# Optimization experiments

Hardware: AMD Instinct MI355X
Metric: run time of the kernel (lower is better)

## Reference

```python
import jax, jax.numpy as jnp
import numpy as np

D_MODEL = 1024
D_STATE = 16
EXPAND = 2
D_INNER = D_MODEL * EXPAND
DT_RANK = D_MODEL // 16


def setup_inputs() -> dict:
    key = jax.random.key(0)
    ks = jax.random.split(key, 12)
    B, T = 2, 2048
    s_in = 1.0 / np.sqrt(D_MODEL)
    s_x = 1.0 / np.sqrt(D_INNER)
    s_dt = 1.0 / np.sqrt(DT_RANK)
    inp = {
        'u': jax.random.normal(ks[0], (B, T, D_MODEL), jnp.float32),
        'W_in': jax.random.uniform(ks[1], (2 * D_INNER, D_MODEL), jnp.float32, -s_in, s_in),
        'b_in': jax.random.uniform(ks[2], (2 * D_INNER,), jnp.float32, -s_in, s_in),
        'W_x': jax.random.uniform(ks[3], (DT_RANK + 2 * D_STATE, D_INNER), jnp.float32, -s_x, s_x),
        'b_x': jax.random.uniform(ks[4], (DT_RANK + 2 * D_STATE,), jnp.float32, -s_x, s_x),
        'W_dt': jax.random.uniform(ks[5], (D_INNER, DT_RANK), jnp.float32, -s_dt, s_dt),
        'b_dt': jax.random.uniform(ks[6], (D_INNER,), jnp.float32, -s_dt, s_dt),
        'A_log': jnp.log(jnp.abs(jax.random.normal(ks[7], (D_INNER, D_STATE), jnp.float32)) + 1e-6),
        'D': jnp.ones((D_INNER,), jnp.float32),
        'W_out': jax.random.uniform(ks[8], (D_MODEL, D_INNER), jnp.float32, -s_x, s_x),
        'b_out': jax.random.uniform(ks[9], (D_MODEL,), jnp.float32, -s_x, s_x),
    }
    return inp


def _ssm_forward(u, W_in, b_in, W_x, b_x, W_dt, b_dt, A_log, D, W_out, b_out):
    B, T, _ = u.shape
    u_inner = u @ W_in.T + b_in                       # [B,T,2*d_inner]
    x, z = jnp.split(u_inner, 2, axis=-1)             # each [B,T,d_inner]
    dbc = x @ W_x.T + b_x                             # [B,T,dt_rank+2N]
    delta_raw = dbc[..., :DT_RANK]
    B_ssm = dbc[..., DT_RANK:DT_RANK + D_STATE]       # [B,T,N]
    C_ssm = dbc[..., DT_RANK + D_STATE:]              # [B,T,N]
    delta = jax.nn.softplus(delta_raw @ W_dt.T + b_dt)  # [B,T,d_inner]
    A = -jnp.exp(A_log)                               # [d_inner,N]

    def step(h, xs):
        dt_t, x_t, Bt, Ct = xs                        # [B,d], [B,d], [B,N], [B,N]
        dA = jnp.exp(dt_t[..., None] * A)             # [B,d,N]
        dB = dt_t[..., None] * Bt[:, None, :]         # [B,d,N]
        h = h * dA + x_t[..., None] * dB
        y_t = jnp.einsum('bdn,bn->bd', h, Ct)
        return h, y_t

    h0 = jnp.zeros((B, D_INNER, D_STATE), u.dtype)
    xs = (jnp.swapaxes(delta, 0, 1), jnp.swapaxes(x, 0, 1),
          jnp.swapaxes(B_ssm, 0, 1), jnp.swapaxes(C_ssm, 0, 1))
    _, y = jax.lax.scan(step, h0, xs)                 # y: [T,B,d_inner]
    y = jnp.swapaxes(y, 0, 1)                         # [B,T,d_inner]
    y = y + x * D
    y = y * (z * jax.nn.sigmoid(z))                   # SiLU gate
    return y @ W_out.T + b_out                        # [B,T,d_model]


def reference(u, W_in, b_in, W_x, b_x, W_dt, b_dt, A_log, D, W_out, b_out):
    return _ssm_forward(u, W_in, b_in, W_x, b_x, W_dt, b_dt, A_log, D, W_out, b_out)
```

## Files before the change

### kernel.cpp

```cpp
#include <hip/hip_runtime.h>
#include <math.h>

#define BATCH 2
#define SEQ   2048
#define DM    1024
#define DI    2048
#define NST   16
#define MT    (BATCH*SEQ)
#define CHK   64
#define LCH   (SEQ/CHK)

typedef __attribute__((ext_vector_type(8))) short  bf16x8;
typedef __attribute__((ext_vector_type(4))) float  f32x4;

static __device__ __forceinline__ unsigned short f2bf(float f) {
  unsigned u = __float_as_uint(f);
  u += 0x7fff + ((u >> 16) & 1);
  return (unsigned short)(u >> 16);
}
static __device__ __forceinline__ float bf2f(unsigned short h) {
  return __uint_as_float(((unsigned)h) << 16);
}
static __device__ __forceinline__ float fexp2(float x) {
  float r;
  asm("v_exp_f32 %0, %1" : "=v"(r) : "v"(x));
  return r;
}
static __device__ __forceinline__ float flog2(float x) {
  float r;
  asm("v_log_f32 %0, %1" : "=v"(r) : "v"(x));
  return r;
}

__global__ __launch_bounds__(256) void conv_bf16_kernel(
    const float* __restrict__ src, unsigned short* __restrict__ dst, int n4)
{
  int i = blockIdx.x * 256 + threadIdx.x;
  if (i < n4) {
    float4 v = ((const float4*)src)[i];
    ushort4 o;
    o.x = f2bf(v.x); o.y = f2bf(v.y); o.z = f2bf(v.z); o.w = f2bf(v.w);
    ((ushort4*)dst)[i] = o;
  }
}

__global__ __launch_bounds__(256) void a2tab_kernel(
    const float* __restrict__ A_log, float* __restrict__ A2tab)
{
  int i = blockIdx.x * 256 + threadIdx.x;
  float4 v = ((const float4*)A_log)[i];
  float4 o;
  o.x = -1.44269504f * __expf(v.x);
  o.y = -1.44269504f * __expf(v.y);
  o.z = -1.44269504f * __expf(v.z);
  o.w = -1.44269504f * __expf(v.w);
  ((float4*)A2tab)[i] = o;
}

template<int BN, bool OUT_BF16, int LDC, int ACT>
__global__ __launch_bounds__(256, 2) void gemm2_kernel(
    const unsigned short* __restrict__ A,
    const unsigned short* __restrict__ B,
    const float* __restrict__ bias,
    void* __restrict__ Cout, int K, int nbx)
{
  constexpr int NJ = BN / 32;
  __shared__ unsigned short Abuf[2][2][128*32];
  __shared__ unsigned short Bbuf[2][2][BN*32];

  const int nwg = gridDim.x;
  const int cpx = nwg >> 3;
  const int bid = blockIdx.x;
  const int swz = (bid & 7) * cpx + (bid >> 3);
  const int bx = swz % nbx;
  const int by = swz / nbx;

  const int tid  = threadIdx.x;
  const int lane = tid & 63;
  const int wid  = tid >> 6;
  const int wr   = wid >> 1;
  const int wc   = wid & 1;
  const int lr    = lane >> 2;
  const int lslot = lane & 3;

  f32x4 zero = {0.f, 0.f, 0.f, 0.f};
  f32x4 acc[4][NJ];
#pragma unroll
  for (int i = 0; i < 4; ++i)
#pragma unroll
    for (int j = 0; j < NJ; ++j) acc[i][j] = zero;

  const size_t arow0 = (size_t)by * 128;
  const size_t brow0 = (size_t)bx * BN;
  const int NT = K >> 6;

  auto STAGE = [&](int buf, int k0) {
#pragma unroll
    for (int half = 0; half < 2; ++half) {
#pragma unroll
      for (int i = 0; i < 2; ++i) {
        const int Rb = (wid + i*4) * 16;
        const int r  = Rb + lr;
        const int c8 = lslot ^ ((r >> 1) & 3);
        const unsigned short* ga = A + (arow0 + r)*(size_t)K + k0 + half*32 + c8*8;
        __builtin_amdgcn_global_load_lds(
            (const __attribute__((address_space(1))) void*)ga,
            (__attribute__((address_space(3))) void*)(&Abuf[buf][half][Rb*32]),
            16, 0, 0);
      }
#pragma unroll
      for (int i = 0; i < BN/64; ++i) {
        const int Rb = (wid + i*4) * 16;
        const int r  = Rb + lr;
        const int c8 = lslot ^ ((r >> 1) & 3);
        const unsigned short* gb = B + (brow0 + r)*(size_t)K + k0 + half*32 + c8*8;
        __builtin_amdgcn_global_load_lds(
            (const __attribute__((address_space(1))) void*)gb,
            (__attribute__((address_space(3))) void*)(&Bbuf[buf][half][Rb*32]),
            16, 0, 0);
      }
    }
  };

  STAGE(0, 0);
  __syncthreads();

  const int lrow = lane & 15, k8 = lane >> 4;
  int cur = 0;
  for (int kt = 0; kt < NT; ++kt) {
    if (kt + 1 < NT) STAGE(cur ^ 1, (kt + 1) * 64);

#pragma unroll
    for (int half = 0; half < 2; ++half) {
      bf16x8 af[4], bfr[NJ];
#pragma unroll
      for (int mi = 0; mi < 4; ++mi) {
        const int r = wr*64 + mi*16 + lrow;
        af[mi] = *(const bf16x8*)&Abuf[cur][half][r*32 + (k8 ^ ((r >> 1) & 3))*8];
      }
#pragma unroll
      for (int nj = 0; nj < NJ; ++nj) {
        const int r = wc*(BN/2) + nj*16 + lrow;
        bfr[nj] = *(const bf16x8*)&Bbuf[cur][half][r*32 + (k8 ^ ((r >> 1) & 3))*8];
      }
      __builtin_amdgcn_s_setprio(1);
#pragma unroll
      for (int mi = 0; mi < 4; ++mi)
#pragma unroll
        for (int nj = 0; nj < NJ; ++nj)
          acc[mi][nj] = __builtin_amdgcn_mfma_f32_16x16x32_bf16(
                            af[mi], bfr[nj], acc[mi][nj], 0, 0, 0);
      __builtin_amdgcn_s_setprio(0);
    }
    __syncthreads();
    cur ^= 1;
  }

  const int lcol = lane & 15, lrq = lane >> 4;
#pragma unroll
  for (int nj = 0; nj < NJ; ++nj) {
    const int colg = bx*BN + wc*(BN/2) + nj*16 + lcol;
    const float bv = bias[colg];
#pragma unroll
    for (int mi = 0; mi < 4; ++mi) {
      const int rowg = by*128 + wr*64 + mi*16 + lrq*4;
#pragma unroll
      for (int q = 0; q < 4; ++q) {
        float v = acc[mi][nj][q] + bv;
        if constexpr (ACT == 1) {
          float e = fexp2(-1.44269504f * fabsf(v));
          v = fmaxf(v, 0.f) + 0.69314718f * flog2(1.f + e);
        }
        if constexpr (OUT_BF16)
          ((unsigned short*)Cout)[(size_t)(rowg + q)*LDC + colg] = f2bf(v);
        else
          ((float*)Cout)[(size_t)(rowg + q)*LDC + colg] = v;
      }
    }
  }
}

__global__ __launch_bounds__(256) void dbc_mfma_kernel(
    const unsigned short* __restrict__ A,
    const unsigned short* __restrict__ Bw,
    const float* __restrict__ bx,
    float* __restrict__ dbc,
    unsigned short* __restrict__ draw_bf)
{
  __shared__ unsigned short Abuf[64*32];
  __shared__ unsigned short Bbuf[96*32];

  const int tid  = threadIdx.x;
  const int lane = tid & 63;
  const int wid  = tid >> 6;
  const int lr    = lane >> 2;
  const int lslot = lane & 3;
  const size_t arow0 = (size_t)blockIdx.x * 64;

  f32x4 zero = {0.f, 0.f, 0.f, 0.f};
  f32x4 acc[6];
#pragma unroll
  for (int j = 0; j < 6; ++j) acc[j] = zero;

  for (int k0 = 0; k0 < DI; k0 += 32) {
    {
      const int Rb = wid*16;
      const int r  = Rb + lr;
      const int c8 = lslot ^ ((r >> 1) & 3);
      const unsigned short* ga = A + (arow0 + r)*4096 + k0 + c8*8;
      __builtin_amdgcn_global_load_lds(
          (const __attribute__((address_space(1))) void*)ga,
          (__attribute__((address_space(3))) void*)(Abuf + Rb*32), 16, 0, 0);
    }
    if (wid < 3) {
#pragma unroll
      for (int i = 0; i < 2; ++i) {
        const int Rb = wid*32 + i*16;
        const int r  = Rb + lr;
        const int c8 = lslot ^ ((r >> 1) & 3);
        const unsigned short* gb = Bw + (size_t)r*DI + k0 + c8*8;
        __builtin_amdgcn_global_load_lds(
            (const __attribute__((address_space(1))) void*)gb,
            (__attribute__((address_space(3))) void*)(Bbuf + Rb*32), 16, 0, 0);
      }
    }
    __syncthreads();

    const int lrow = lane & 15, k8 = lane >> 4;
    const int ra = wid*16 + lrow;
    bf16x8 af = *(const bf16x8*)&Abuf[ra*32 + (k8 ^ ((ra >> 1) & 3))*8];
#pragma unroll
    for (int nj = 0; nj < 6; ++nj) {
      const int rb = nj*16 + lrow;
      bf16x8 bf_ = *(const bf16x8*)&Bbuf[rb*32 + (k8 ^ ((rb >> 1) & 3))*8];
      acc[nj] = __builtin_amdgcn_mfma_f32_16x16x32_bf16(af, bf_, acc[nj], 0, 0, 0);
    }
    __syncthreads();
  }

  const int lcol = lane & 15, lrq = lane >> 4;
  const int rowg = (int)arow0 + wid*16 + lrq*4;
#pragma unroll
  for (int nj = 0; nj < 6; ++nj) {
    const int colg = nj*16 + lcol;
    const float bv = bx[colg];
#pragma unroll
    for (int q = 0; q < 4; ++q) {
      float v = acc[nj][q] + bv;
      if (nj < 4)
        draw_bf[(size_t)(rowg + q)*64 + colg] = f2bf(v);
      else
        dbc[(size_t)(rowg + q)*96 + colg] = v;
    }
  }
}

__global__ __launch_bounds__(256) void scanA_kernel(
    const unsigned short* __restrict__ uib,
    const float* __restrict__ dbc,
    const unsigned short* __restrict__ delta_bf,
    const float* __restrict__ A2tab,
    float* __restrict__ P,
    float* __restrict__ S)
{
  const int bid = blockIdx.x;
  const int d   = (bid & 7)*256 + threadIdx.x;
  const int c   = (bid >> 3) & (CHK-1);
  const int b   = bid >> 9;

  float A2[NST];
  {
    const float4* ap = (const float4*)(A2tab + (size_t)d*NST);
#pragma unroll
    for (int q = 0; q < 4; ++q) {
      float4 v = ap[q];
      A2[q*4+0] = v.x; A2[q*4+1] = v.y; A2[q*4+2] = v.z; A2[q*4+3] = v.w;
    }
  }

  float h[NST];
#pragma unroll
  for (int nn = 0; nn < NST; ++nn) h[nn] = 0.f;
  float sdt = 0.f;

  const int t0 = c * LCH;
  const unsigned short* dptr = delta_bf + ((size_t)b*SEQ + t0)*DI + d;
  const unsigned short* xptr = uib      + ((size_t)b*SEQ + t0)*4096 + d;
  const float* bptr          = dbc      + ((size_t)b*SEQ + t0)*96 + 64;

  float dt = bf2f(dptr[0]);
  float xv = bf2f(xptr[0]);
  float4 Bv0 = *(const float4*)(bptr + 0);
  float4 Bv1 = *(const float4*)(bptr + 4);
  float4 Bv2 = *(const float4*)(bptr + 8);
  float4 Bv3 = *(const float4*)(bptr + 12);

  for (int t = 0; t < LCH; ++t) {
    const float dtc = dt, xvc = xv;
    float Bc[NST] = {Bv0.x,Bv0.y,Bv0.z,Bv0.w, Bv1.x,Bv1.y,Bv1.z,Bv1.w,
                     Bv2.x,Bv2.y,Bv2.z,Bv2.w, Bv3.x,Bv3.y,Bv3.z,Bv3.w};
    if (t + 1 < LCH) {
      const size_t tn = (size_t)(t+1);
      dt = bf2f(dptr[tn*DI]);
      xv = bf2f(xptr[tn*4096]);
      const float* bp = bptr + tn*96;
      Bv0 = *(const float4*)(bp + 0);
      Bv1 = *(const float4*)(bp + 4);
      Bv2 = *(const float4*)(bp + 8);
      Bv3 = *(const float4*)(bp + 12);
    }
    sdt += dtc;
    const float xdt = xvc * dtc;
#pragma unroll
    for (int nn = 0; nn < NST; ++nn) {
      float dA = fexp2(dtc * A2[nn]);
      h[nn] = h[nn]*dA + xdt*Bc[nn];
    }
  }

  float* Pp = P + (((size_t)b*CHK + c)*DI + d)*NST;
  float* Sp = S + (((size_t)b*CHK + c)*DI + d)*NST;
#pragma unroll
  for (int q = 0; q < 4; ++q) {
    float4 pv = { fexp2(A2[q*4+0]*sdt), fexp2(A2[q*4+1]*sdt),
                  fexp2(A2[q*4+2]*sdt), fexp2(A2[q*4+3]*sdt) };
    float4 sv = { h[q*4+0], h[q*4+1], h[q*4+2], h[q*4+3] };
    *(float4*)(Pp + q*4) = pv;
    *(float4*)(Sp + q*4) = sv;
  }
}

__global__ __launch_bounds__(256) void scanB_kernel(
    const float* __restrict__ P, float* __restrict__ S)
{
  const int gid = blockIdx.x*256 + threadIdx.x;
  const int n4 = gid & 3;
  const int d  = (gid >> 2) & (DI-1);
  const int b  = gid >> 13;

  float4 h = {0.f, 0.f, 0.f, 0.f};
  for (int c = 0; c < CHK; ++c) {
    const size_t idx = (((size_t)b*CHK + c)*DI + d)*NST + n4*4;
    float4 p = *(const float4*)(P + idx);
    float4 s = *(const float4*)(S + idx);
    *(float4*)(S + idx) = h;
    h.x = h.x*p.x + s.x;
    h.y = h.y*p.y + s.y;
    h.z = h.z*p.z + s.z;
    h.w = h.w*p.w + s.w;
  }
}

__global__ __launch_bounds__(256) void scanC_kernel(
    const unsigned short* __restrict__ uib,
    const float* __restrict__ dbc,
    const unsigned short* __restrict__ delta_bf,
    const float* __restrict__ A2tab,
    const float* __restrict__ Dp,
    const float* __restrict__ S,
    unsigned short* __restrict__ y_bf)
{
  const int bid = blockIdx.x;
  const int d   = (bid & 7)*256 + threadIdx.x;
  const int c   = (bid >> 3) & (CHK-1);
  const int b   = bid >> 9;

  float A2[NST];
  {
    const float4* ap = (const float4*)(A2tab + (size_t)d*NST);
#pragma unroll
    for (int q = 0; q < 4; ++q) {
      float4 v = ap[q];
      A2[q*4+0] = v.x; A2[q*4+1] = v.y; A2[q*4+2] = v.z; A2[q*4+3] = v.w;
    }
  }
  const float Dv = Dp[d];

  float h[NST];
  {
    const float* Sp = S + (((size_t)b*CHK + c)*DI + d)*NST;
#pragma unroll
    for (int q = 0; q < 4; ++q) {
      float4 sv = *(const float4*)(Sp + q*4);
      h[q*4+0] = sv.x; h[q*4+1] = sv.y; h[q*4+2] = sv.z; h[q*4+3] = sv.w;
    }
  }

  const int t0 = c * LCH;
  const unsigned short* dptr = delta_bf + ((size_t)b*SEQ + t0)*DI + d;
  const unsigned short* xptr = uib      + ((size_t)b*SEQ + t0)*4096 + d;
  const float* cptr          = dbc      + ((size_t)b*SEQ + t0)*96;
  unsigned short* yp         = y_bf     + ((size_t)b*SEQ + t0)*DI + d;

  float dt = bf2f(dptr[0]);
  float xv = bf2f(xptr[0]);
  float zv = bf2f(xptr[2048]);
  float4 Bv0 = *(const float4*)(cptr + 64);
  float4 Bv1 = *(const float4*)(cptr + 68);
  float4 Bv2 = *(const float4*)(cptr + 72);
  float4 Bv3 = *(const float4*)(cptr + 76);
  float4 Cv0 = *(const float4*)(cptr + 80);
  float4 Cv1 = *(const float4*)(cptr + 84);
  float4 Cv2 = *(const float4*)(cptr + 88);
  float4 Cv3 = *(const float4*)(cptr + 92);

  for (int t = 0; t < LCH; ++t) {
    const float dtc = dt, xvc = xv, zvc = zv;
    float Bc[NST] = {Bv0.x,Bv0.y,Bv0.z,Bv0.w, Bv1.x,Bv1.y,Bv1.z,Bv1.w,
                     Bv2.x,Bv2.y,Bv2.z,Bv2.w, Bv3.x,Bv3.y,Bv3.z,Bv3.w};
    float Cc[NST] = {Cv0.x,Cv0.y,Cv0.z,Cv0.w, Cv1.x,Cv1.y,Cv1.z,Cv1.w,
                     Cv2.x,Cv2.y,Cv2.z,Cv2.w, Cv3.x,Cv3.y,Cv3.z,Cv3.w};
    if (t + 1 < LCH) {
      const size_t tn = (size_t)(t+1);
      dt = bf2f(dptr[tn*DI]);
      xv = bf2f(xptr[tn*4096]);
      zv = bf2f(xptr[tn*4096 + 2048]);
      const float* cp = cptr + tn*96;
      Bv0 = *(const float4*)(cp + 64);
      Bv1 = *(const float4*)(cp + 68);
      Bv2 = *(const float4*)(cp + 72);
      Bv3 = *(const float4*)(cp + 76);
      Cv0 = *(const float4*)(cp + 80);
      Cv1 = *(const float4*)(cp + 84);
      Cv2 = *(const float4*)(cp + 88);
      Cv3 = *(const float4*)(cp + 92);
    }
    const float xdt = xvc * dtc;
    float y = 0.f;
#pragma unroll
    for (int nn = 0; nn < NST; ++nn) {
      float dA = fexp2(dtc * A2[nn]);
      h[nn] = h[nn]*dA + xdt*Bc[nn];
      y += h[nn]*Cc[nn];
    }
    y += xvc * Dv;
    y *= zvc / (1.f + fexp2(-1.44269504f * zvc));
    yp[(size_t)t*DI] = f2bf(y);
  }
}

extern "C" void kernel_launch(void* const* d_in, const int* in_sizes, int n_in,
                              void* d_out, int out_size, void* d_ws, size_t ws_size,
                              hipStream_t stream)
{
  const float* u     = (const float*)d_in[0];
  const float* W_in  = (const float*)d_in[1];
  const float* b_in  = (const float*)d_in[2];
  const float* W_x   = (const float*)d_in[3];
  const float* b_x   = (const float*)d_in[4];
  const float* W_dt  = (const float*)d_in[5];
  const float* b_dt  = (const float*)d_in[6];
  const float* A_log = (const float*)d_in[7];
  const float* Dp    = (const float*)d_in[8];
  const float* W_out = (const float*)d_in[9];
  const float* b_out = (const float*)d_in[10];
  float* out = (float*)d_out;

  unsigned short* ui_bf    = (unsigned short*)d_ws;
  float*          dbc      = (float*)(ui_bf + (size_t)MT*4096);
  unsigned short* delta_bf = (unsigned short*)(dbc + (size_t)MT*96);
  unsigned short* y_bf     = delta_bf + (size_t)MT*DI;
  unsigned short* wout_bf  = y_bf + (size_t)MT*DI;
  unsigned short* wx_bf    = wout_bf + (size_t)DM*DI;
  unsigned short* wdt_bf   = wx_bf + (size_t)96*DI;
  unsigned short* draw_bf  = wdt_bf + (size_t)DI*64;
  float*          S        = (float*)(draw_bf + (size_t)MT*64);
  float*          A2tab    = S + (size_t)BATCH*CHK*DI*NST;

  unsigned short* u_bf   = (unsigned short*)d_out;
  unsigned short* win_bf = u_bf + (size_t)MT*DM;
  float* P = (float*)d_out;

  conv_bf16_kernel<<<4096, 256, 0, stream>>>(u,     u_bf,    MT*DM/4);
  conv_bf16_kernel<<<4096, 256, 0, stream>>>(W_in,  win_bf,  2*DI*DM/4);
  conv_bf16_kernel<<<2048, 256, 0, stream>>>(W_out, wout_bf, DM*DI/4);
  conv_bf16_kernel<<<192,  256, 0, stream>>>(W_x,   wx_bf,   96*DI/4);
  conv_bf16_kernel<<<128,  256, 0, stream>>>(W_dt,  wdt_bf,  DI*64/4);
  a2tab_kernel<<<DI*NST/1024, 256, 0, stream>>>(A_log, A2tab);

  gemm2_kernel<128, true, 4096, 0><<<32*32, 256, 0, stream>>>(
      u_bf, win_bf, b_in, ui_bf, DM, 32);

  dbc_mfma_kernel<<<MT/64, 256, 0, stream>>>(ui_bf, wx_bf, b_x, dbc, draw_bf);

  gemm2_kernel<128, true, 2048, 1><<<16*32, 256, 0, stream>>>(
      draw_bf, wdt_bf, b_dt, delta_bf, 64, 16);

  scanA_kernel<<<BATCH*CHK*DI/256, 256, 0, stream>>>(ui_bf, dbc, delta_bf, A2tab, P, S);
  scanB_kernel<<<BATCH*DI*4/256, 256, 0, stream>>>(P, S);
  scanC_kernel<<<BATCH*CHK*DI/256, 256, 0, stream>>>(ui_bf, dbc, delta_bf, A2tab, Dp, S, y_bf);

  gemm2_kernel<64, false, 1024, 0><<<16*32, 256, 0, stream>>>(
      y_bf, wout_bf, b_out, out, DI, 16);
}
```

Baseline: 215.4 us.

## Fuse conversion kernels, split-K the dbc GEMM, and tune GEMM K-tile and occupancy

The five bf16 conversion launches and the A2 table launch are merged into one kernel that branches on a global index range. The dbc projection GEMM is split four ways along K into a partial buffer, followed by a reduce kernel that adds the bias and writes the outputs, so more workgroups run. The generic GEMM gains a BK template parameter: the in-projection and delta GEMMs use BK=32 to shrink shared memory, and launch bounds rise to 4 waves per SIMD. This trades an extra launch and a partial-sum round trip for more parallelism, and risks register spills from the tighter occupancy bound.

```diff
diff --git a/kernel.cpp b/kernel.cpp
--- a/kernel.cpp
+++ b/kernel.cpp
@@ -32,41 +32,62 @@
   return r;
 }
 
-__global__ __launch_bounds__(256) void conv_bf16_kernel(
-    const float* __restrict__ src, unsigned short* __restrict__ dst, int n4)
-{
-  int i = blockIdx.x * 256 + threadIdx.x;
-  if (i < n4) {
-    float4 v = ((const float4*)src)[i];
-    ushort4 o;
-    o.x = f2bf(v.x); o.y = f2bf(v.y); o.z = f2bf(v.z); o.w = f2bf(v.w);
-    ((ushort4*)dst)[i] = o;
-  }
-}
-
-__global__ __launch_bounds__(256) void a2tab_kernel(
-    const float* __restrict__ A_log, float* __restrict__ A2tab)
-{
-  int i = blockIdx.x * 256 + threadIdx.x;
-  float4 v = ((const float4*)A_log)[i];
-  float4 o;
-  o.x = -1.44269504f * __expf(v.x);
-  o.y = -1.44269504f * __expf(v.y);
-  o.z = -1.44269504f * __expf(v.z);
-  o.w = -1.44269504f * __expf(v.w);
-  ((float4*)A2tab)[i] = o;
-}
-
-template<int BN, bool OUT_BF16, int LDC, int ACT>
-__global__ __launch_bounds__(256, 2) void gemm2_kernel(
+#define SEG_U    (MT*DM/4)
+#define SEG_WIN  (2*DI*DM/4)
+#define SEG_WOUT (DM*DI/4)
+#define SEG_WX   (96*DI/4)
+#define SEG_WDT  (DI*64/4)
+#define SEG_A    (DI*NST/4)
+#define CUM0 SEG_U
+#define CUM1 (CUM0+SEG_WIN)
+#define CUM2 (CUM1+SEG_WOUT)
+#define CUM3 (CUM2+SEG_WX)
+#define CUM4 (CUM3+SEG_WDT)
+#define CUM5 (CUM4+SEG_A)
+
+__global__ __launch_bounds__(256) void convall_kernel(
+    const float* __restrict__ u, const float* __restrict__ W_in,
+    const float* __restrict__ W_out, const float* __restrict__ W_x,
+    const float* __restrict__ W_dt, const float* __restrict__ A_log,
+    unsigned short* __restrict__ u_bf, unsigned short* __restrict__ win_bf,
+    unsigned short* __restrict__ wout_bf, unsigned short* __restrict__ wx_bf,
+    unsigned short* __restrict__ wdt_bf, float* __restrict__ A2tab)
+{
+  const int gid = blockIdx.x*256 + threadIdx.x;
+  const float4* src; ushort4* dst; int idx;
+  if (gid < CUM0)      { idx = gid;        src = (const float4*)u;     dst = (ushort4*)u_bf; }
+  else if (gid < CUM1) { idx = gid - CUM0; src = (const float4*)W_in;  dst = (ushort4*)win_bf; }
+  else if (gid < CUM2) { idx = gid - CUM1; src = (const float4*)W_out; dst = (ushort4*)wout_bf; }
+  else if (gid < CUM3) { idx = gid - CUM2; src = (const float4*)W_x;   dst = (ushort4*)wx_bf; }
+  else if (gid < CUM4) { idx = gid - CUM3; src = (const float4*)W_dt;  dst = (ushort4*)wdt_bf; }
+  else if (gid < CUM5) {
+    int i = gid - CUM4;
+    float4 v = ((const float4*)A_log)[i];
+    float4 o;
+    o.x = -1.44269504f * __expf(v.x);
+    o.y = -1.44269504f * __expf(v.y);
+    o.z = -1.44269504f * __expf(v.z);
+    o.w = -1.44269504f * __expf(v.w);
+    ((float4*)A2tab)[i] = o;
+    return;
+  } else return;
+  float4 v = src[idx];
+  ushort4 o;
+  o.x = f2bf(v.x); o.y = f2bf(v.y); o.z = f2bf(v.z); o.w = f2bf(v.w);
+  dst[idx] = o;
+}
+
+template<int BN, int BK, bool OUT_BF16, int LDC, int ACT>
+__global__ __launch_bounds__(256, 4) void gemm2_kernel(
     const unsigned short* __restrict__ A,
     const unsigned short* __restrict__ B,
     const float* __restrict__ bias,
     void* __restrict__ Cout, int K, int nbx)
 {
+  constexpr int NH = BK / 32;
   constexpr int NJ = BN / 32;
-  __shared__ unsigned short Abuf[2][2][128*32];
-  __shared__ unsigned short Bbuf[2][2][BN*32];
+  __shared__ unsigned short Abuf[2][NH][128*32];
+  __shared__ unsigned short Bbuf[2][NH][BN*32];
 
   const int nwg = gridDim.x;
   const int cpx = nwg >> 3;
@@ -92,11 +113,11 @@
 
   const size_t arow0 = (size_t)by * 128;
   const size_t brow0 = (size_t)bx * BN;
-  const int NT = K >> 6;
+  const int NT = K / BK;
 
   auto STAGE = [&](int buf, int k0) {
 #pragma unroll
-    for (int half = 0; half < 2; ++half) {
+    for (int half = 0; half < NH; ++half) {
 #pragma unroll
       for (int i = 0; i < 2; ++i) {
         const int Rb = (wid + i*4) * 16;
@@ -128,10 +149,10 @@
   const int lrow = lane & 15, k8 = lane >> 4;
   int cur = 0;
   for (int kt = 0; kt < NT; ++kt) {
-    if (kt + 1 < NT) STAGE(cur ^ 1, (kt + 1) * 64);
-
-#pragma unroll
-    for (int half = 0; half < 2; ++half) {
+    if (kt + 1 < NT) STAGE(cur ^ 1, (kt + 1) * BK);
+
+#pragma unroll
+    for (int half = 0; half < NH; ++half) {
       bf16x8 af[4], bfr[NJ];
 #pragma unroll
       for (int mi = 0; mi < 4; ++mi) {
@@ -183,9 +204,7 @@
 __global__ __launch_bounds__(256) void dbc_mfma_kernel(
     const unsigned short* __restrict__ A,
     const unsigned short* __restrict__ Bw,
-    const float* __restrict__ bx,
-    float* __restrict__ dbc,
-    unsigned short* __restrict__ draw_bf)
+    float* __restrict__ partial)
 {
   __shared__ unsigned short Abuf[64*32];
   __shared__ unsigned short Bbuf[96*32];
@@ -196,13 +215,15 @@
   const int lr    = lane >> 2;
   const int lslot = lane & 3;
   const size_t arow0 = (size_t)blockIdx.x * 64;
+  const int ks   = blockIdx.y;
+  const int k0b  = ks * (DI/4);
 
   f32x4 zero = {0.f, 0.f, 0.f, 0.f};
   f32x4 acc[6];
 #pragma unroll
   for (int j = 0; j < 6; ++j) acc[j] = zero;
 
-  for (int k0 = 0; k0 < DI; k0 += 32) {
+  for (int k0 = k0b; k0 < k0b + DI/4; k0 += 32) {
     {
       const int Rb = wid*16;
       const int r  = Rb + lr;
@@ -243,16 +264,24 @@
 #pragma unroll
   for (int nj = 0; nj < 6; ++nj) {
     const int colg = nj*16 + lcol;
-    const float bv = bx[colg];
-#pragma unroll
-    for (int q = 0; q < 4; ++q) {
-      float v = acc[nj][q] + bv;
-      if (nj < 4)
-        draw_bf[(size_t)(rowg + q)*64 + colg] = f2bf(v);
-      else
-        dbc[(size_t)(rowg + q)*96 + colg] = v;
-    }
-  }
+#pragma unroll
+    for (int q = 0; q < 4; ++q)
+      partial[((size_t)ks*MT + rowg + q)*96 + colg] = acc[nj][q];
+  }
+}
+
+__global__ __launch_bounds__(256) void dbc_reduce_kernel(
+    const float* __restrict__ partial, const float* __restrict__ bx,
+    float* __restrict__ dbc, unsigned short* __restrict__ draw_bf)
+{
+  const int gid = blockIdx.x*256 + threadIdx.x;
+  const int m = gid / 96;
+  const int c = gid - m*96;
+  const size_t stride = (size_t)MT*96;
+  float s = partial[gid] + partial[gid + stride]
+          + partial[gid + 2*stride] + partial[gid + 3*stride] + bx[c];
+  if (c < 64) draw_bf[(size_t)m*64 + c] = f2bf(s);
+  else        dbc[(size_t)m*96 + c] = s;
 }
 
 __global__ __launch_bounds__(256) void scanA_kernel(
@@ -466,30 +495,29 @@
   unsigned short* draw_bf  = wdt_bf + (size_t)DI*64;
   float*          S        = (float*)(draw_bf + (size_t)MT*64);
   float*          A2tab    = S + (size_t)BATCH*CHK*DI*NST;
+  float*          partial  = A2tab + (size_t)DI*NST;
 
   unsigned short* u_bf   = (unsigned short*)d_out;
   unsigned short* win_bf = u_bf + (size_t)MT*DM;
   float* P = (float*)d_out;
 
-  conv_bf16_kernel<<<4096, 256, 0, stream>>>(u,     u_bf,    MT*DM/4);
-  conv_bf16_kernel<<<4096, 256, 0, stream>>>(W_in,  win_bf,  2*DI*DM/4);
-  conv_bf16_kernel<<<2048, 256, 0, stream>>>(W_out, wout_bf, DM*DI/4);
-  conv_bf16_kernel<<<192,  256, 0, stream>>>(W_x,   wx_bf,   96*DI/4);
-  conv_bf16_kernel<<<128,  256, 0, stream>>>(W_dt,  wdt_bf,  DI*64/4);
-  a2tab_kernel<<<DI*NST/1024, 256, 0, stream>>>(A_log, A2tab);
-
-  gemm2_kernel<128, true, 4096, 0><<<32*32, 256, 0, stream>>>(
+  convall_kernel<<<CUM5/256, 256, 0, stream>>>(
+      u, W_in, W_out, W_x, W_dt, A_log,
+      u_bf, win_bf, wout_bf, wx_bf, wdt_bf, A2tab);
+
+  gemm2_kernel<128, 32, true, 4096, 0><<<32*32, 256, 0, stream>>>(
       u_bf, win_bf, b_in, ui_bf, DM, 32);
 
-  dbc_mfma_kernel<<<MT/64, 256, 0, stream>>>(ui_bf, wx_bf, b_x, dbc, draw_bf);
-
-  gemm2_kernel<128, true, 2048, 1><<<16*32, 256, 0, stream>>>(
+  dbc_mfma_kernel<<<dim3(MT/64, 4), 256, 0, stream>>>(ui_bf, wx_bf, partial);
+  dbc_reduce_kernel<<<MT*96/256, 256, 0, stream>>>(partial, b_x, dbc, draw_bf);
+
+  gemm2_kernel<128, 32, true, 2048, 1><<<16*32, 256, 0, stream>>>(
       draw_bf, wdt_bf, b_dt, delta_bf, 64, 16);
 
   scanA_kernel<<<BATCH*CHK*DI/256, 256, 0, stream>>>(ui_bf, dbc, delta_bf, A2tab, P, S);
   scanB_kernel<<<BATCH*DI*4/256, 256, 0, stream>>>(P, S);
   scanC_kernel<<<BATCH*CHK*DI/256, 256, 0, stream>>>(ui_bf, dbc, delta_bf, A2tab, Dp, S, y_bf);
 
-  gemm2_kernel<64, false, 1024, 0><<<16*32, 256, 0, stream>>>(
+  gemm2_kernel<64, 64, false, 1024, 0><<<16*32, 256, 0, stream>>>(
       y_bf, wout_bf, b_out, out, DI, 16);
 }
```

Result: faster. 185.2 us (-14.0%).
